# Kernel optimization log

Measured on AMD Instinct MI355X. Metric: run time of the kernel, lower is better.

The kernel has to match this reference:

```python
import jax, jax.numpy as jnp
import numpy as np

N = 100000      # num_nodes
E = 1600000     # num_edges
D_IN = 256      # input_dim
H = 64          # hidden_dim
OUT = 32        # output_dim
EMB = 128       # node2vec embedding_dim
HEADS = 2       # GAT heads (concat=False -> mean over heads)
NEG_SLOPE = 0.2 # GATConv leaky_relu default


def setup_inputs() -> dict:
    key = jax.random.key(0)
    ks = jax.random.split(key, 24)
    s = lambda k, shape, fan: (jax.random.normal(k, shape, jnp.float32) * (1.0 / np.sqrt(fan)))
    return {
        "x": jax.random.normal(ks[0], (N, D_IN), jnp.float32),
        "edge_index": jax.random.randint(ks[1], (2, E), 0, N, jnp.int64),
        # frozen node2vec embedding table (used under no_grad in the original)
        "n2v_emb": jax.random.normal(ks[2], (N, EMB), jnp.float32),
        "n2v_proj_w": s(ks[3], (EMB, H), EMB), "n2v_proj_b": jnp.zeros((H,), jnp.float32),
        "input_proj_w": s(ks[4], (D_IN + H, H), D_IN + H), "input_proj_b": jnp.zeros((H,), jnp.float32),
        "gate_w": s(ks[5], (D_IN + H, H), D_IN + H), "gate_b": jnp.zeros((H,), jnp.float32),
        # SAGEConv layers: out = mean_agg(x_j) @ wl + bl + x @ wr
        "sage0_wl": s(ks[6], (H, H), H), "sage0_bl": jnp.zeros((H,), jnp.float32), "sage0_wr": s(ks[7], (H, H), H),
        "sage1_wl": s(ks[8], (H, H), H), "sage1_bl": jnp.zeros((H,), jnp.float32), "sage1_wr": s(ks[9], (H, H), H),
        # GATConv(H, H, heads=2, concat=False)
        "gat_w": s(ks[10], (H, HEADS * H), H),
        "gat_att_src": s(ks[11], (HEADS, H), H), "gat_att_dst": s(ks[12], (HEADS, H), H),
        "gat_b": jnp.zeros((H,), jnp.float32),
        "fin_wl": s(ks[13], (H, OUT), H), "fin_bl": jnp.zeros((OUT,), jnp.float32), "fin_wr": s(ks[14], (H, OUT), H),
    }


def _sage(h, src, dst, wl, bl, wr, n):
    # PyG SAGEConv with mean aggregation: lin_l(mean_j h_j) + lin_r(h_i)
    msum = jax.ops.segment_sum(h[src], dst, num_segments=n)
    deg = jax.ops.segment_sum(jnp.ones((src.shape[0],), h.dtype), dst, num_segments=n)
    agg = msum / jnp.maximum(deg, 1.0)[:, None]
    return agg @ wl + bl + h @ wr


def _gat(h, src, dst, w, att_src, att_dst, b, n):
    # GATConv with self-loops (PyG default), heads averaged (concat=False)
    loops = jnp.arange(n, dtype=src.dtype)
    src = jnp.concatenate([src, loops]); dst = jnp.concatenate([dst, loops])
    xh = (h @ w).reshape(n, HEADS, H)                     # [n, heads, H]
    a_src = jnp.einsum('nhd,hd->nh', xh, att_src)         # [n, heads]
    a_dst = jnp.einsum('nhd,hd->nh', xh, att_dst)
    e = jax.nn.leaky_relu(a_src[src] + a_dst[dst], NEG_SLOPE)  # [E', heads]
    emax = jax.ops.segment_max(e, dst, num_segments=n)
    ex = jnp.exp(e - emax[dst])
    esum = jax.ops.segment_sum(ex, dst, num_segments=n)
    alpha = ex / (esum[dst] + 1e-16)                      # edge softmax per dst, per head
    out = jax.ops.segment_sum(alpha[:, :, None] * xh[src], dst, num_segments=n)
    return out.mean(axis=1) + b                           # [n, H]


def reference(x, edge_index, n2v_emb, n2v_proj_w, n2v_proj_b, input_proj_w, input_proj_b,
              gate_w, gate_b, sage0_wl, sage0_bl, sage0_wr, sage1_wl, sage1_bl, sage1_wr,
              gat_w, gat_att_src, gat_att_dst, gat_b, fin_wl, fin_bl, fin_wr):
    n = x.shape[0]
    src, dst = edge_index[0], edge_index[1]
    # node2vec embeddings are frozen (torch.no_grad in original)
    n2v = jax.lax.stop_gradient(n2v_emb)
    n2v_p = n2v @ n2v_proj_w + n2v_proj_b                 # [n, H]
    combined = jnp.concatenate([x, n2v_p], axis=-1)       # [n, D_IN+H]
    gate = jax.nn.sigmoid(combined @ gate_w + gate_b)
    x_proj = combined @ input_proj_w + input_proj_b
    raw_proj = jnp.concatenate([x, jnp.zeros((n, H), x.dtype)], axis=-1) @ input_proj_w + input_proj_b
    h = gate * x_proj + (1.0 - gate) * raw_proj           # node_indices=None -> all nodes
    h = jax.nn.relu(_sage(h, src, dst, sage0_wl, sage0_bl, sage0_wr, n))
    h = jax.nn.relu(_sage(h, src, dst, sage1_wl, sage1_bl, sage1_wr, n))
    h = jax.nn.relu(_gat(h, src, dst, gat_w, gat_att_src, gat_att_dst, gat_b, n))
    return _sage(h, src, dst, fin_wl, fin_bl, fin_wr, n)  # [n, OUT]
```

## Files before the change

kernel.cpp:

```cpp
#include <hip/hip_runtime.h>
#include <math.h>

#define NN 100000
#define NE 1600000
#define DIN 256
#define HD 64
#define OUTD 32
#define EMBD 128
#define SLOPE 0.2f
#define AST 68
#define NT ((NN + 63) / 64)
#define SCHUNK 1024
#define SNBLK ((NN + SCHUNK - 1) / SCHUNK)
#define FCH 25000
#define FNC ((NE + FCH - 1) / FCH)

typedef __attribute__((ext_vector_type(8))) short bf16x8;
typedef __attribute__((ext_vector_type(8))) unsigned short u16x8;
typedef __attribute__((ext_vector_type(4))) float f32x4;

__device__ __forceinline__ float lrelu(float x) { return x > 0.f ? x : SLOPE * x; }
__device__ __forceinline__ ushort f2b(float f) {
    unsigned u = __float_as_uint(f);
    return (ushort)((u + 0x7FFFu + ((u >> 16) & 1u)) >> 16);
}
__device__ __forceinline__ float b2f(ushort v) { return __uint_as_float(((unsigned)v) << 16); }

__global__ void k_count(const int* __restrict__ dst, int* __restrict__ cnt) {
    int i = blockIdx.x * blockDim.x + threadIdx.x;
    if (i < NE) atomicAdd(&cnt[dst[i]], 1);
}

__global__ __launch_bounds__(256) void k_scan1(const int* __restrict__ cnt,
                                               int* __restrict__ rowptr,
                                               int* __restrict__ blksum) {
    __shared__ int ts[256];
    int base = blockIdx.x * SCHUNK + threadIdx.x * 4;
    int v0 = 0, v1 = 0, v2 = 0, v3 = 0;
    if (base < NN)     v0 = cnt[base];
    if (base + 1 < NN) v1 = cnt[base + 1];
    if (base + 2 < NN) v2 = cnt[base + 2];
    if (base + 3 < NN) v3 = cnt[base + 3];
    int s = v0 + v1 + v2 + v3;
    ts[threadIdx.x] = s;
    __syncthreads();
    for (int off = 1; off < 256; off <<= 1) {
        int w = (threadIdx.x >= off) ? ts[threadIdx.x - off] : 0;
        __syncthreads();
        ts[threadIdx.x] += w;
        __syncthreads();
    }
    int excl = ts[threadIdx.x] - s;
    if (base < NN)     rowptr[base]     = excl;
    if (base + 1 < NN) rowptr[base + 1] = excl + v0;
    if (base + 2 < NN) rowptr[base + 2] = excl + v0 + v1;
    if (base + 3 < NN) rowptr[base + 3] = excl + v0 + v1 + v2;
    if (threadIdx.x == 255) blksum[blockIdx.x] = ts[255];
}

__global__ __launch_bounds__(128) void k_scan2(int* __restrict__ blksum) {
    __shared__ int ts[128];
    int t = threadIdx.x;
    int v = (t < SNBLK) ? blksum[t] : 0;
    ts[t] = v;
    __syncthreads();
    for (int off = 1; off < 128; off <<= 1) {
        int w = (t >= off) ? ts[t - off] : 0;
        __syncthreads();
        ts[t] += w;
        __syncthreads();
    }
    if (t < SNBLK) blksum[t] = ts[t] - v;
}

__global__ void k_scan3(const int* __restrict__ blksum, const int* __restrict__ cnt,
                        int* __restrict__ rowptr, int* __restrict__ cursor,
                        float* __restrict__ invdeg) {
    int i = blockIdx.x * blockDim.x + threadIdx.x;
    if (i < NN) {
        int v = rowptr[i] + blksum[i >> 10];
        rowptr[i] = v;
        cursor[i] = v;
        invdeg[i] = 1.0f / fmaxf((float)cnt[i], 1.0f);
    }
    if (i == 0) rowptr[NN] = NE;
}

__global__ __launch_bounds__(256) void k_fill_x(const int* __restrict__ src,
                                                const int* __restrict__ dst,
                                                int* __restrict__ cursor,
                                                int* __restrict__ colsrc) {
    int xcd = blockIdx.x & 7;
    int chunk = blockIdx.x >> 3;
    int lo = xcd * (NN / 8);
    int hi = (xcd == 7) ? NN : lo + (NN / 8);
    int beg = chunk * FCH;
    int end = min(beg + FCH, NE);
    for (int i = beg + (int)threadIdx.x; i < end; i += 256) {
        int d = dst[i];
        if (d >= lo && d < hi) {
            int pos = atomicAdd(&cursor[d], 1);
            colsrc[pos] = src[i];
        }
    }
}

__device__ __forceinline__ void stageA(const float* __restrict__ g, int nbase, int ldg, int koff,
                                       float (*As)[AST]) {
    for (int i = threadIdx.x; i < 1024; i += 256) {
        int m = i >> 4, k4 = (i & 15) << 2;
        int row = nbase + m;
        if (row >= NN) row = NN - 1;
        *(float4*)&As[m][k4] = *(const float4*)&g[(size_t)row * ldg + koff + k4];
    }
}
__device__ __forceinline__ void stageW(const float* __restrict__ g, float* Ws) {
    for (int i = threadIdx.x; i < 1024; i += 256) ((float4*)Ws)[i] = ((const float4*)g)[i];
}
__device__ __forceinline__ void stageWcols(const float* __restrict__ g, int ldg, int coff,
                                           float* Ws) {
    for (int i = threadIdx.x; i < 1024; i += 256) {
        int r = i >> 4, c4 = (i & 15) << 2;
        *(float4*)&Ws[r * 64 + c4] = *(const float4*)&g[r * ldg + coff + c4];
    }
}
__device__ __forceinline__ void mac16v(const float (*As)[AST], const float* __restrict__ Ws,
                                       float (*acc)[4], int tr, int tc) {
#pragma unroll 4
    for (int k4 = 0; k4 < 64; k4 += 4) {
        float4 a0 = *(const float4*)&As[tr * 4 + 0][k4];
        float4 a1 = *(const float4*)&As[tr * 4 + 1][k4];
        float4 a2 = *(const float4*)&As[tr * 4 + 2][k4];
        float4 a3 = *(const float4*)&As[tr * 4 + 3][k4];
#pragma unroll
        for (int j = 0; j < 4; j++) {
            float4 w = *(const float4*)&Ws[(k4 + j) * 64 + tc * 4];
            float e0 = (&a0.x)[j], e1 = (&a1.x)[j], e2 = (&a2.x)[j], e3 = (&a3.x)[j];
            acc[0][0] += e0 * w.x; acc[0][1] += e0 * w.y; acc[0][2] += e0 * w.z; acc[0][3] += e0 * w.w;
            acc[1][0] += e1 * w.x; acc[1][1] += e1 * w.y; acc[1][2] += e1 * w.z; acc[1][3] += e1 * w.w;
            acc[2][0] += e2 * w.x; acc[2][1] += e2 * w.y; acc[2][2] += e2 * w.z; acc[2][3] += e2 * w.w;
            acc[3][0] += e3 * w.x; acc[3][1] += e3 * w.y; acc[3][2] += e3 * w.z; acc[3][3] += e3 * w.w;
        }
    }
}

__global__ __launch_bounds__(256) void k_n2vp_t(const float* __restrict__ n2v,
                                                const float* __restrict__ w,
                                                const float* __restrict__ b,
                                                float* __restrict__ n2vp) {
    __shared__ float As[64][AST];
    __shared__ float Ws[64 * 64];
    int nbase = blockIdx.x * 64;
    int tc = threadIdx.x & 15, tr = threadIdx.x >> 4;
    float acc[4][4] = {};
    for (int c = 0; c < 2; c++) {
        if (c) __syncthreads();
        stageA(n2v, nbase, EMBD, c * 64, As);
        stageW(w + c * 64 * 64, Ws);
        __syncthreads();
        mac16v(As, Ws, acc, tr, tc);
    }
    float b0 = b[tc * 4], b1 = b[tc * 4 + 1], b2 = b[tc * 4 + 2], b3 = b[tc * 4 + 3];
#pragma unroll
    for (int i = 0; i < 4; i++) {
        int row = nbase + tr * 4 + i;
        if (row < NN) {
            float4 o = {acc[i][0] + b0, acc[i][1] + b1, acc[i][2] + b2, acc[i][3] + b3};
            *(float4*)&n2vp[(size_t)row * HD + tc * 4] = o;
        }
    }
}

__global__ __launch_bounds__(256) void k_front_t(const float* __restrict__ x,
                                                 const float* __restrict__ n2vp,
                                                 const float* __restrict__ ip_w,
                                                 const float* __restrict__ ip_b,
                                                 const float* __restrict__ gate_w,
                                                 const float* __restrict__ gate_b,
                                                 float* __restrict__ h0,
                                                 ushort* __restrict__ h0b) {
    __shared__ ushort Ah[64][40], Al[64][40];
    __shared__ ushort Bih[64][40], Bil[64][40];
    __shared__ ushort Bgh[64][40], Bgl[64][40];
    int nbase = blockIdx.x * 64;
    int tid = threadIdx.x;
    int w = tid >> 6, l = tid & 63;
    int lr = l & 15, lg = l >> 4, lk = lg * 8;
    f32x4 zero = {0.f, 0.f, 0.f, 0.f};
    f32x4 araw[4], ag[4], adel[4];
#pragma unroll
    for (int t = 0; t < 4; t++) { araw[t] = zero; ag[t] = zero; adel[t] = zero; }

    int arow = tid >> 2, ak0 = (tid & 3) << 3;
    int garow = nbase + arow;
    if (garow >= NN) garow = NN - 1;

    for (int c = 0; c < 8; c++) {
        if (c) __syncthreads();
        {
            const float* src = &x[(size_t)garow * DIN + c * 32 + ak0];
            u16x8 th, tl;
#pragma unroll
            for (int u = 0; u < 8; u++) {
                float v = src[u];
                ushort h = f2b(v);
                th[u] = h;
                tl[u] = f2b(v - b2f(h));
            }
            *(u16x8*)&Ah[arow][ak0] = th;
            *(u16x8*)&Al[arow][ak0] = tl;
        }
        {
            const float* pi = &ip_w[(size_t)(c * 32 + w * 8) * 64 + l];
            const float* pg = &gate_w[(size_t)(c * 32 + w * 8) * 64 + l];
            u16x8 ih, il, gh, gl2;
#pragma unroll
            for (int u = 0; u < 8; u++) {
                float v = pi[u * 64];
                ushort h = f2b(v);
                ih[u] = h; il[u] = f2b(v - b2f(h));
                float g = pg[u * 64];
                ushort hg = f2b(g);
                gh[u] = hg; gl2[u] = f2b(g - b2f(hg));
            }
            *(u16x8*)&Bih[l][w * 8] = ih;
            *(u16x8*)&Bil[l][w * 8] = il;
            *(u16x8*)&Bgh[l][w * 8] = gh;
            *(u16x8*)&Bgl[l][w * 8] = gl2;
        }
        __syncthreads();
        bf16x8 ah = *(const bf16x8*)&Ah[w * 16 + lr][lk];
        bf16x8 al = *(const bf16x8*)&Al[w * 16 + lr][lk];
#pragma unroll
        for (int t = 0; t < 4; t++) {
            int col = t * 16 + lr;
            bf16x8 bih = *(const bf16x8*)&Bih[col][lk];
            bf16x8 bil = *(const bf16x8*)&Bil[col][lk];
            bf16x8 bgh = *(const bf16x8*)&Bgh[col][lk];
            bf16x8 bgl = *(const bf16x8*)&Bgl[col][lk];
            f32x4 r = araw[t];
            r = __builtin_amdgcn_mfma_f32_16x16x32_bf16(ah, bih, r, 0, 0, 0);
            r = __builtin_amdgcn_mfma_f32_16x16x32_bf16(ah, bil, r, 0, 0, 0);
            r = __builtin_amdgcn_mfma_f32_16x16x32_bf16(al, bih, r, 0, 0, 0);
            araw[t] = r;
            f32x4 g = ag[t];
            g = __builtin_amdgcn_mfma_f32_16x16x32_bf16(ah, bgh, g, 0, 0, 0);
            g = __builtin_amdgcn_mfma_f32_16x16x32_bf16(ah, bgl, g, 0, 0, 0);
            g = __builtin_amdgcn_mfma_f32_16x16x32_bf16(al, bgh, g, 0, 0, 0);
            ag[t] = g;
        }
    }
    for (int c = 0; c < 2; c++) {
        __syncthreads();
        {
            const float* src = &n2vp[(size_t)garow * HD + c * 32 + ak0];
            u16x8 th, tl;
#pragma unroll
            for (int u = 0; u < 8; u++) {
                float v = src[u];
                ushort h = f2b(v);
                th[u] = h;
                tl[u] = f2b(v - b2f(h));
            }
            *(u16x8*)&Ah[arow][ak0] = th;
            *(u16x8*)&Al[arow][ak0] = tl;
        }
        {
            const float* pi = &ip_w[(size_t)(DIN + c * 32 + w * 8) * 64 + l];
            const float* pg = &gate_w[(size_t)(DIN + c * 32 + w * 8) * 64 + l];
            u16x8 ih, il, gh, gl2;
#pragma unroll
            for (int u = 0; u < 8; u++) {
                float v = pi[u * 64];
                ushort h = f2b(v);
                ih[u] = h; il[u] = f2b(v - b2f(h));
                float g = pg[u * 64];
                ushort hg = f2b(g);
                gh[u] = hg; gl2[u] = f2b(g - b2f(hg));
            }
            *(u16x8*)&Bih[l][w * 8] = ih;
            *(u16x8*)&Bil[l][w * 8] = il;
            *(u16x8*)&Bgh[l][w * 8] = gh;
            *(u16x8*)&Bgl[l][w * 8] = gl2;
        }
        __syncthreads();
        bf16x8 ah = *(const bf16x8*)&Ah[w * 16 + lr][lk];
        bf16x8 al = *(const bf16x8*)&Al[w * 16 + lr][lk];
#pragma unroll
        for (int t = 0; t < 4; t++) {
            int col = t * 16 + lr;
            bf16x8 bih = *(const bf16x8*)&Bih[col][lk];
            bf16x8 bil = *(const bf16x8*)&Bil[col][lk];
            bf16x8 bgh = *(const bf16x8*)&Bgh[col][lk];
            bf16x8 bgl = *(const bf16x8*)&Bgl[col][lk];
            f32x4 r = adel[t];
            r = __builtin_amdgcn_mfma_f32_16x16x32_bf16(ah, bih, r, 0, 0, 0);
            r = __builtin_amdgcn_mfma_f32_16x16x32_bf16(ah, bil, r, 0, 0, 0);
            r = __builtin_amdgcn_mfma_f32_16x16x32_bf16(al, bih, r, 0, 0, 0);
            adel[t] = r;
            f32x4 g = ag[t];
            g = __builtin_amdgcn_mfma_f32_16x16x32_bf16(ah, bgh, g, 0, 0, 0);
            g = __builtin_amdgcn_mfma_f32_16x16x32_bf16(ah, bgl, g, 0, 0, 0);
            g = __builtin_amdgcn_mfma_f32_16x16x32_bf16(al, bgh, g, 0, 0, 0);
            ag[t] = g;
        }
    }
#pragma unroll
    for (int t = 0; t < 4; t++) {
        int col = t * 16 + lr;
        float ib = ip_b[col], gb2 = gate_b[col];
#pragma unroll
        for (int r = 0; r < 4; r++) {
            int row = nbase + w * 16 + lg * 4 + r;
            if (row < NN) {
                float raw = araw[t][r] + ib;
                float sg = 1.f / (1.f + __expf(-(ag[t][r] + gb2)));
                float o = raw + sg * adel[t][r];
                h0[(size_t)row * HD + col] = o;
                h0b[(size_t)row * HD + col] = f2b(o);
            }
        }
    }
}

__global__ void k_gather_mean(const int* __restrict__ rowptr, const int* __restrict__ colsrc,
                              const float* __restrict__ invdeg, const ushort* __restrict__ hb,
                              float* __restrict__ agg) {
    int t = threadIdx.x & 63;
    int lane = t & 31, half = t >> 5;
    int gw = blockIdx.x * (blockDim.x >> 6) + (threadIdx.x >> 6);
    int stride = gridDim.x * (blockDim.x >> 6);
    for (int n = gw; n < NN; n += stride) {
        int bg = rowptr[n], en = rowptr[n + 1];
        float a0 = 0.f, a1 = 0.f;
        int i = bg + half;
        for (; i + 6 < en; i += 8) {
            int sa = colsrc[i], sb = colsrc[i + 2], sc = colsrc[i + 4], sd = colsrc[i + 6];
            ushort2 va = *(const ushort2*)&hb[(size_t)sa * HD + lane * 2];
            ushort2 vb = *(const ushort2*)&hb[(size_t)sb * HD + lane * 2];
            ushort2 vc = *(const ushort2*)&hb[(size_t)sc * HD + lane * 2];
            ushort2 vd = *(const ushort2*)&hb[(size_t)sd * HD + lane * 2];
            a0 += b2f(va.x) + b2f(vb.x) + b2f(vc.x) + b2f(vd.x);
            a1 += b2f(va.y) + b2f(vb.y) + b2f(vc.y) + b2f(vd.y);
        }
        for (; i < en; i += 2) {
            int s = colsrc[i];
            ushort2 v = *(const ushort2*)&hb[(size_t)s * HD + lane * 2];
            a0 += b2f(v.x);
            a1 += b2f(v.y);
        }
        a0 += __shfl_xor(a0, 32);
        a1 += __shfl_xor(a1, 32);
        if (half == 0) {
            float id = invdeg[n];
            float2 o = {a0 * id, a1 * id};
            *(float2*)&agg[(size_t)n * HD + lane * 2] = o;
        }
    }
}

__global__ __launch_bounds__(256) void k_sage_t(const float* __restrict__ agg,
                                                const float* __restrict__ h,
                                                const float* __restrict__ wl,
                                                const float* __restrict__ bl,
                                                const float* __restrict__ wr,
                                                float* __restrict__ hout,
                                                ushort* __restrict__ houtb) {
    __shared__ float As[64][AST];
    __shared__ float Ws[64 * 64];
    int nbase = blockIdx.x * 64;
    int tc = threadIdx.x & 15, tr = threadIdx.x >> 4;
    float acc[4][4] = {};
    stageA(agg, nbase, HD, 0, As);
    stageW(wl, Ws);
    __syncthreads();
    mac16v(As, Ws, acc, tr, tc);
    __syncthreads();
    stageA(h, nbase, HD, 0, As);
    stageW(wr, Ws);
    __syncthreads();
    mac16v(As, Ws, acc, tr, tc);
    float b0 = bl[tc * 4], b1 = bl[tc * 4 + 1], b2 = bl[tc * 4 + 2], b3 = bl[tc * 4 + 3];
#pragma unroll
    for (int i = 0; i < 4; i++) {
        int row = nbase + tr * 4 + i;
        if (row < NN) {
            float4 o = {fmaxf(acc[i][0] + b0, 0.f), fmaxf(acc[i][1] + b1, 0.f),
                        fmaxf(acc[i][2] + b2, 0.f), fmaxf(acc[i][3] + b3, 0.f)};
            *(float4*)&hout[(size_t)row * HD + tc * 4] = o;
            ushort4 ob = {f2b(o.x), f2b(o.y), f2b(o.z), f2b(o.w)};
            *(ushort4*)&houtb[(size_t)row * HD + tc * 4] = ob;
        }
    }
}

__global__ __launch_bounds__(256) void k_gatxh_t(const float* __restrict__ h,
                                                 const float* __restrict__ w,
                                                 const float* __restrict__ att_s,
                                                 const float* __restrict__ att_d,
                                                 ushort* __restrict__ xhb,
                                                 float* __restrict__ a_s,
                                                 float* __restrict__ a_d) {
    __shared__ float As[64][AST];
    __shared__ float Ws[64 * 64];
    int nbase = blockIdx.x * 64;
    int tc = threadIdx.x & 15, tr = threadIdx.x >> 4;
    stageA(h, nbase, HD, 0, As);
#pragma unroll
    for (int half = 0; half < 2; half++) {
        if (half) __syncthreads();
        stageWcols(w, 128, half * 64, Ws);
        __syncthreads();
        float acc[4][4] = {};
        mac16v(As, Ws, acc, tr, tc);
        float as0 = att_s[half * 64 + tc * 4], as1 = att_s[half * 64 + tc * 4 + 1];
        float as2 = att_s[half * 64 + tc * 4 + 2], as3 = att_s[half * 64 + tc * 4 + 3];
        float ad0 = att_d[half * 64 + tc * 4], ad1 = att_d[half * 64 + tc * 4 + 1];
        float ad2 = att_d[half * 64 + tc * 4 + 2], ad3 = att_d[half * 64 + tc * 4 + 3];
#pragma unroll
        for (int i = 0; i < 4; i++) {
            int row = nbase + tr * 4 + i;
            float ps = acc[i][0] * as0 + acc[i][1] * as1 + acc[i][2] * as2 + acc[i][3] * as3;
            float pd = acc[i][0] * ad0 + acc[i][1] * ad1 + acc[i][2] * ad2 + acc[i][3] * ad3;
#pragma unroll
            for (int off = 8; off; off >>= 1) {
                ps += __shfl_xor(ps, off);
                pd += __shfl_xor(pd, off);
            }
            if (row < NN) {
                ushort4 ob = {f2b(acc[i][0]), f2b(acc[i][1]), f2b(acc[i][2]), f2b(acc[i][3])};
                *(ushort4*)&xhb[(size_t)row * 128 + half * 64 + tc * 4] = ob;
                if (tc == 0) {
                    a_s[row * 2 + half] = ps;
                    a_d[row * 2 + half] = pd;
                }
            }
        }
    }
}

__global__ void k_gat_fused(const int* __restrict__ rowptr, const int* __restrict__ colsrc,
                            const float* __restrict__ a_s, const float* __restrict__ a_d,
                            const ushort* __restrict__ xhb, const float* __restrict__ gb,
                            float* __restrict__ hout) {
    int t = threadIdx.x & 63;
    int lane = t & 31, half = t >> 5;
    int bl4 = (lane & 15) * 4;
    float4 bias4 = *(const float4*)&gb[bl4];
    int gw = blockIdx.x * (blockDim.x >> 6) + (threadIdx.x >> 6);
    int stride = gridDim.x * (blockDim.x >> 6);
    for (int n = gw; n < NN; n += stride) {
        int bg = rowptr[n], en = rowptr[n + 1];
        float ad0 = a_d[n * 2], ad1 = a_d[n * 2 + 1];
        float a0 = 0.f, a1 = 0.f, a2 = 0.f, a3 = 0.f;
        float ss0 = 0.f, ss1 = 0.f;
        int i = bg + half;
        for (; i + 2 < en; i += 4) {
            int sa = colsrc[i], sb = colsrc[i + 2];
            float2 ava = *(const float2*)&a_s[sa * 2];
            float2 avb = *(const float2*)&a_s[sb * 2];
            ushort4 xva = *(const ushort4*)&xhb[(size_t)sa * 128 + lane * 4];
            ushort4 xvb = *(const ushort4*)&xhb[(size_t)sb * 128 + lane * 4];
            float wa0 = __expf(lrelu(ava.x + ad0));
            float wa1 = __expf(lrelu(ava.y + ad1));
            float wb0 = __expf(lrelu(avb.x + ad0));
            float wb1 = __expf(lrelu(avb.y + ad1));
            ss0 += wa0 + wb0;
            ss1 += wa1 + wb1;
            float wsa = (lane < 16) ? wa0 : wa1;
            float wsb = (lane < 16) ? wb0 : wb1;
            a0 += wsa * b2f(xva.x) + wsb * b2f(xvb.x);
            a1 += wsa * b2f(xva.y) + wsb * b2f(xvb.y);
            a2 += wsa * b2f(xva.z) + wsb * b2f(xvb.z);
            a3 += wsa * b2f(xva.w) + wsb * b2f(xvb.w);
        }
        for (; i < en; i += 2) {
            int s = colsrc[i];
            float2 av = *(const float2*)&a_s[s * 2];
            float w0 = __expf(lrelu(av.x + ad0));
            float w1 = __expf(lrelu(av.y + ad1));
            ss0 += w0;
            ss1 += w1;
            float wsel = (lane < 16) ? w0 : w1;
            ushort4 xv = *(const ushort4*)&xhb[(size_t)s * 128 + lane * 4];
            a0 += wsel * b2f(xv.x);
            a1 += wsel * b2f(xv.y);
            a2 += wsel * b2f(xv.z);
            a3 += wsel * b2f(xv.w);
        }
        if (half == 0) {
            float2 av = *(const float2*)&a_s[n * 2];
            float w0 = __expf(lrelu(av.x + ad0));
            float w1 = __expf(lrelu(av.y + ad1));
            ss0 += w0;
            ss1 += w1;
            float wsel = (lane < 16) ? w0 : w1;
            ushort4 xv = *(const ushort4*)&xhb[(size_t)n * 128 + lane * 4];
            a0 += wsel * b2f(xv.x);
            a1 += wsel * b2f(xv.y);
            a2 += wsel * b2f(xv.z);
            a3 += wsel * b2f(xv.w);
        }
        ss0 += __shfl_xor(ss0, 32);
        ss1 += __shfl_xor(ss1, 32);
        a0 += __shfl_xor(a0, 32);
        a1 += __shfl_xor(a1, 32);
        a2 += __shfl_xor(a2, 32);
        a3 += __shfl_xor(a3, 32);
        float r = (lane < 16) ? (0.5f / (ss0 + 1e-16f)) : (0.5f / (ss1 + 1e-16f));
        float v0 = a0 * r, v1 = a1 * r, v2 = a2 * r, v3 = a3 * r;
        float p0 = __shfl_xor(v0, 16);
        float p1 = __shfl_xor(v1, 16);
        float p2 = __shfl_xor(v2, 16);
        float p3 = __shfl_xor(v3, 16);
        if (half == 0 && lane < 16) {
            float4 o = {fmaxf(v0 + p0 + bias4.x, 0.f), fmaxf(v1 + p1 + bias4.y, 0.f),
                        fmaxf(v2 + p2 + bias4.z, 0.f), fmaxf(v3 + p3 + bias4.w, 0.f)};
            *(float4*)&hout[(size_t)n * HD + lane * 4] = o;
        }
    }
}

__global__ void k_pfin(const float* __restrict__ h, const float* __restrict__ wl,
                       ushort* __restrict__ Pb) {
    __shared__ float sw[HD * OUTD];
    for (int i = threadIdx.x; i < HD * OUTD; i += blockDim.x) sw[i] = wl[i];
    __syncthreads();
    int t = threadIdx.x & 63;
    int c = t & 31, half = t >> 5;
    int gw = blockIdx.x * (blockDim.x >> 6) + (threadIdx.x >> 6);
    int stride = gridDim.x * (blockDim.x >> 6);
    for (int n = gw; n < NN; n += stride) {
        float hv = h[(size_t)n * HD + t];
        float acc = 0.f;
#pragma unroll 8
        for (int i = 0; i < 32; i++) {
            float bb = __shfl(hv, half * 32 + i);
            acc += bb * sw[half * 1024 + i * 32 + c];
        }
        acc += __shfl_xor(acc, 32);
        if (half == 0) Pb[(size_t)n * OUTD + c] = f2b(acc);
    }
}

__global__ void k_final_fused(const int* __restrict__ rowptr, const int* __restrict__ colsrc,
                              const float* __restrict__ invdeg, const ushort* __restrict__ Pb,
                              const float* __restrict__ h, const float* __restrict__ bl,
                              const float* __restrict__ wr, float* __restrict__ out) {
    __shared__ float sw[HD * OUTD];
    for (int i = threadIdx.x; i < HD * OUTD; i += blockDim.x) sw[i] = wr[i];
    __syncthreads();
    int t = threadIdx.x & 63;
    int j = t & 31, half = t >> 5;
    int quarter = t >> 4, lane16 = t & 15;
    float bias = bl[j];
    int gw = blockIdx.x * (blockDim.x >> 6) + (threadIdx.x >> 6);
    int stride = gridDim.x * (blockDim.x >> 6);
    for (int n = gw; n < NN; n += stride) {
        int bg = rowptr[n], en = rowptr[n + 1];
        float a0 = 0.f, a1 = 0.f;
        int i = bg + quarter;
        for (; i + 4 < en; i += 8) {
            int sa = colsrc[i], sb = colsrc[i + 4];
            ushort2 va = *(const ushort2*)&Pb[(size_t)sa * OUTD + lane16 * 2];
            ushort2 vb = *(const ushort2*)&Pb[(size_t)sb * OUTD + lane16 * 2];
            a0 += b2f(va.x) + b2f(vb.x);
            a1 += b2f(va.y) + b2f(vb.y);
        }
        for (; i < en; i += 4) {
            int s = colsrc[i];
            ushort2 v = *(const ushort2*)&Pb[(size_t)s * OUTD + lane16 * 2];
            a0 += b2f(v.x);
            a1 += b2f(v.y);
        }
        a0 += __shfl_xor(a0, 32);
        a1 += __shfl_xor(a1, 32);
        a0 += __shfl_xor(a0, 16);
        a1 += __shfl_xor(a1, 16);
        float hv = h[(size_t)n * HD + t];
        float o = 0.f;
#pragma unroll 8
        for (int i2 = 0; i2 < 32; i2++) {
            float bb = __shfl(hv, half * 32 + i2);
            o += bb * sw[half * 1024 + i2 * 32 + j];
        }
        o += __shfl_xor(o, 32);
        float ga = __shfl(a0, j >> 1);
        float gb_ = __shfl(a1, j >> 1);
        float gv = (j & 1) ? gb_ : ga;
        if (half == 0) out[(size_t)n * OUTD + j] = gv * invdeg[n] + bias + o;
    }
}

extern "C" void kernel_launch(void* const* d_in, const int* in_sizes, int n_in,
                              void* d_out, int out_size, void* d_ws, size_t ws_size,
                              hipStream_t stream) {
    const float* x      = (const float*)d_in[0];
    const int*   eidx   = (const int*)d_in[1];
    const float* n2v    = (const float*)d_in[2];
    const float* n2v_w  = (const float*)d_in[3];
    const float* n2v_b  = (const float*)d_in[4];
    const float* ip_w   = (const float*)d_in[5];
    const float* ip_b   = (const float*)d_in[6];
    const float* gate_w = (const float*)d_in[7];
    const float* gate_b = (const float*)d_in[8];
    const float* s0_wl  = (const float*)d_in[9];
    const float* s0_bl  = (const float*)d_in[10];
    const float* s0_wr  = (const float*)d_in[11];
    const float* s1_wl  = (const float*)d_in[12];
    const float* s1_bl  = (const float*)d_in[13];
    const float* s1_wr  = (const float*)d_in[14];
    const float* gat_w  = (const float*)d_in[15];
    const float* att_s  = (const float*)d_in[16];
    const float* att_d  = (const float*)d_in[17];
    const float* gat_b  = (const float*)d_in[18];
    const float* f_wl   = (const float*)d_in[19];
    const float* f_bl   = (const float*)d_in[20];
    const float* f_wr   = (const float*)d_in[21];

    const int* src = eidx;
    const int* dst = eidx + NE;

    float*  ws     = (float*)d_ws;
    float*  invdeg = ws;
    float*  S1     = invdeg + NN;
    float*  S2     = S1 + (size_t)NN * HD;
    float*  SA     = S2 + (size_t)NN * HD;
    float*  a_s    = SA + (size_t)NN * HD;
    float*  a_d    = a_s + (size_t)NN * 2;
    ushort* Pb     = (ushort*)(a_d + (size_t)NN * 2);
    ushort* hb     = Pb + (size_t)NN * OUTD;
    ushort* xhb    = hb + (size_t)NN * HD;
    int*    cnt    = (int*)(xhb + (size_t)NN * 128);
    int*    rowptr = cnt + NN;
    int*    cursor = rowptr + NN + 1;
    int*    blksum = cursor + NN;
    int*    colsrc = blksum + 128;

    float* n2vp = SA;
    float* agg  = SA;
    float* out  = (float*)d_out;

    const int BT = 256;
    dim3 b128(128), b256(BT);
    int eblk = (NE + BT - 1) / BT;
    int nblk = (NN + BT - 1) / BT;

    hipMemsetAsync(cnt, 0, (size_t)NN * 4, stream);
    k_count<<<eblk, b256, 0, stream>>>(dst, cnt);
    k_scan1<<<SNBLK, b256, 0, stream>>>(cnt, rowptr, blksum);
    k_scan2<<<1, b128, 0, stream>>>(blksum);
    k_scan3<<<nblk, b256, 0, stream>>>(blksum, cnt, rowptr, cursor, invdeg);
    k_fill_x<<<8 * FNC, b256, 0, stream>>>(src, dst, cursor, colsrc);

    k_n2vp_t<<<NT, b256, 0, stream>>>(n2v, n2v_w, n2v_b, n2vp);
    k_front_t<<<NT, b256, 0, stream>>>(x, n2vp, ip_w, ip_b, gate_w, gate_b, S2, hb);

    k_gather_mean<<<2048, b256, 0, stream>>>(rowptr, colsrc, invdeg, hb, agg);
    k_sage_t<<<NT, b256, 0, stream>>>(agg, S2, s0_wl, s0_bl, s0_wr, S1, hb);

    k_gather_mean<<<2048, b256, 0, stream>>>(rowptr, colsrc, invdeg, hb, agg);
    k_sage_t<<<NT, b256, 0, stream>>>(agg, S1, s1_wl, s1_bl, s1_wr, S2, hb);

    k_gatxh_t<<<NT, b256, 0, stream>>>(S2, gat_w, att_s, att_d, xhb, a_s, a_d);
    k_gat_fused<<<2048, b256, 0, stream>>>(rowptr, colsrc, a_s, a_d, xhb, gat_b, S1);

    k_pfin<<<2048, b256, 0, stream>>>(S1, f_wl, Pb);
    k_final_fused<<<2048, b256, 0, stream>>>(rowptr, colsrc, invdeg, Pb, S1, f_bl, f_wr, out);
}
```

Measured before the change: 695.7 us.

## Fuse node2vec projection and CSR fill into a single front kernel launch

Removes the separate n2v projection kernel by computing it with split-bf16 MFMA inside the front kernel and keeping the result in registers. That result is then staged straight into shared memory, so the n2vp intermediate is never written to or read back from global memory. The CSR fill blocks are appended to the same grid, so the atomic scatter can overlap with the front-end GEMM work and one launch is saved. The costs are extra registers for the held projection and a precision change from fp32 FMA to three-term bf16 MFMA for the projection.

```diff
diff --git a/kernel.cpp b/kernel.cpp
--- a/kernel.cpp
+++ b/kernel.cpp
@@ -86,25 +86,6 @@
     if (i == 0) rowptr[NN] = NE;
 }
 
-__global__ __launch_bounds__(256) void k_fill_x(const int* __restrict__ src,
-                                                const int* __restrict__ dst,
-                                                int* __restrict__ cursor,
-                                                int* __restrict__ colsrc) {
-    int xcd = blockIdx.x & 7;
-    int chunk = blockIdx.x >> 3;
-    int lo = xcd * (NN / 8);
-    int hi = (xcd == 7) ? NN : lo + (NN / 8);
-    int beg = chunk * FCH;
-    int end = min(beg + FCH, NE);
-    for (int i = beg + (int)threadIdx.x; i < end; i += 256) {
-        int d = dst[i];
-        if (d >= lo && d < hi) {
-            int pos = atomicAdd(&cursor[d], 1);
-            colsrc[pos] = src[i];
-        }
-    }
-}
-
 __device__ __forceinline__ void stageA(const float* __restrict__ g, int nbase, int ldg, int koff,
                                        float (*As)[AST]) {
     for (int i = threadIdx.x; i < 1024; i += 256) {
@@ -144,65 +125,107 @@
     }
 }
 
-__global__ __launch_bounds__(256) void k_n2vp_t(const float* __restrict__ n2v,
-                                                const float* __restrict__ w,
-                                                const float* __restrict__ b,
-                                                float* __restrict__ n2vp) {
-    __shared__ float As[64][AST];
-    __shared__ float Ws[64 * 64];
-    int nbase = blockIdx.x * 64;
-    int tc = threadIdx.x & 15, tr = threadIdx.x >> 4;
-    float acc[4][4] = {};
-    for (int c = 0; c < 2; c++) {
-        if (c) __syncthreads();
-        stageA(n2v, nbase, EMBD, c * 64, As);
-        stageW(w + c * 64 * 64, Ws);
-        __syncthreads();
-        mac16v(As, Ws, acc, tr, tc);
-    }
-    float b0 = b[tc * 4], b1 = b[tc * 4 + 1], b2 = b[tc * 4 + 2], b3 = b[tc * 4 + 3];
-#pragma unroll
-    for (int i = 0; i < 4; i++) {
-        int row = nbase + tr * 4 + i;
-        if (row < NN) {
-            float4 o = {acc[i][0] + b0, acc[i][1] + b1, acc[i][2] + b2, acc[i][3] + b3};
-            *(float4*)&n2vp[(size_t)row * HD + tc * 4] = o;
-        }
-    }
-}
-
-__global__ __launch_bounds__(256) void k_front_t(const float* __restrict__ x,
-                                                 const float* __restrict__ n2vp,
-                                                 const float* __restrict__ ip_w,
-                                                 const float* __restrict__ ip_b,
-                                                 const float* __restrict__ gate_w,
-                                                 const float* __restrict__ gate_b,
-                                                 float* __restrict__ h0,
-                                                 ushort* __restrict__ h0b) {
+__global__ __launch_bounds__(256) void k_megafront(
+        const float* __restrict__ x, const float* __restrict__ n2v,
+        const float* __restrict__ n2v_w, const float* __restrict__ n2v_b,
+        const float* __restrict__ ip_w, const float* __restrict__ ip_b,
+        const float* __restrict__ gate_w, const float* __restrict__ gate_b,
+        float* __restrict__ h0, ushort* __restrict__ h0b,
+        const int* __restrict__ esrc, const int* __restrict__ edst,
+        int* __restrict__ cursor, int* __restrict__ colsrc) {
     __shared__ ushort Ah[64][40], Al[64][40];
     __shared__ ushort Bih[64][40], Bil[64][40];
     __shared__ ushort Bgh[64][40], Bgl[64][40];
+
+    if (blockIdx.x >= NT) {
+        int fb = blockIdx.x - NT;
+        int cls = blockIdx.x & 7;
+        int chunk = fb >> 3;
+        int lo = cls * (NN / 8);
+        int hi = (cls == 7) ? NN : lo + (NN / 8);
+        int beg = chunk * FCH;
+        int end = min(beg + FCH, NE);
+        for (int i = beg + (int)threadIdx.x; i < end; i += 256) {
+            int d = edst[i];
+            if (d >= lo && d < hi) {
+                int pos = atomicAdd(&cursor[d], 1);
+                colsrc[pos] = esrc[i];
+            }
+        }
+        return;
+    }
+
     int nbase = blockIdx.x * 64;
     int tid = threadIdx.x;
     int w = tid >> 6, l = tid & 63;
     int lr = l & 15, lg = l >> 4, lk = lg * 8;
     f32x4 zero = {0.f, 0.f, 0.f, 0.f};
-    f32x4 araw[4], ag[4], adel[4];
-#pragma unroll
-    for (int t = 0; t < 4; t++) { araw[t] = zero; ag[t] = zero; adel[t] = zero; }
+    f32x4 araw[4], ag[4], adel[4], pn[4];
+#pragma unroll
+    for (int t = 0; t < 4; t++) { araw[t] = zero; ag[t] = zero; adel[t] = zero; pn[t] = zero; }
 
     int arow = tid >> 2, ak0 = (tid & 3) << 3;
     int garow = nbase + arow;
     if (garow >= NN) garow = NN - 1;
 
-    for (int c = 0; c < 8; c++) {
+    for (int c = 0; c < 4; c++) {
         if (c) __syncthreads();
         {
-            const float* src = &x[(size_t)garow * DIN + c * 32 + ak0];
+            const float* ap = &n2v[(size_t)garow * EMBD + c * 32 + ak0];
             u16x8 th, tl;
 #pragma unroll
             for (int u = 0; u < 8; u++) {
-                float v = src[u];
+                float v = ap[u];
+                ushort h = f2b(v);
+                th[u] = h;
+                tl[u] = f2b(v - b2f(h));
+            }
+            *(u16x8*)&Ah[arow][ak0] = th;
+            *(u16x8*)&Al[arow][ak0] = tl;
+        }
+        {
+            const float* pw = &n2v_w[(size_t)(c * 32 + w * 8) * 64 + l];
+            u16x8 ih, il;
+#pragma unroll
+            for (int u = 0; u < 8; u++) {
+                float v = pw[u * 64];
+                ushort h = f2b(v);
+                ih[u] = h;
+                il[u] = f2b(v - b2f(h));
+            }
+            *(u16x8*)&Bih[l][w * 8] = ih;
+            *(u16x8*)&Bil[l][w * 8] = il;
+        }
+        __syncthreads();
+        bf16x8 ah = *(const bf16x8*)&Ah[w * 16 + lr][lk];
+        bf16x8 al = *(const bf16x8*)&Al[w * 16 + lr][lk];
+#pragma unroll
+        for (int t = 0; t < 4; t++) {
+            int col = t * 16 + lr;
+            bf16x8 bih = *(const bf16x8*)&Bih[col][lk];
+            bf16x8 bil = *(const bf16x8*)&Bil[col][lk];
+            f32x4 r = pn[t];
+            r = __builtin_amdgcn_mfma_f32_16x16x32_bf16(ah, bih, r, 0, 0, 0);
+            r = __builtin_amdgcn_mfma_f32_16x16x32_bf16(ah, bil, r, 0, 0, 0);
+            r = __builtin_amdgcn_mfma_f32_16x16x32_bf16(al, bih, r, 0, 0, 0);
+            pn[t] = r;
+        }
+    }
+#pragma unroll
+    for (int t = 0; t < 4; t++) {
+        float nb = n2v_b[t * 16 + lr];
+#pragma unroll
+        for (int r = 0; r < 4; r++) pn[t][r] += nb;
+    }
+
+    for (int c = 0; c < 8; c++) {
+        __syncthreads();
+        {
+            const float* ap = &x[(size_t)garow * DIN + c * 32 + ak0];
+            u16x8 th, tl;
+#pragma unroll
+            for (int u = 0; u < 8; u++) {
+                float v = ap[u];
                 ushort h = f2b(v);
                 th[u] = h;
                 tl[u] = f2b(v - b2f(h));
@@ -250,20 +273,21 @@
             ag[t] = g;
         }
     }
+
     for (int c = 0; c < 2; c++) {
         __syncthreads();
-        {
-            const float* src = &n2vp[(size_t)garow * HD + c * 32 + ak0];
-            u16x8 th, tl;
-#pragma unroll
-            for (int u = 0; u < 8; u++) {
-                float v = src[u];
+#pragma unroll
+        for (int tt = 0; tt < 2; tt++) {
+            int t = c * 2 + tt;
+            int ak = tt * 16 + lr;
+#pragma unroll
+            for (int r = 0; r < 4; r++) {
+                int row = w * 16 + lg * 4 + r;
+                float v = pn[t][r];
                 ushort h = f2b(v);
-                th[u] = h;
-                tl[u] = f2b(v - b2f(h));
-            }
-            *(u16x8*)&Ah[arow][ak0] = th;
-            *(u16x8*)&Al[arow][ak0] = tl;
+                Ah[row][ak] = h;
+                Al[row][ak] = f2b(v - b2f(h));
+            }
         }
         {
             const float* pi = &ip_w[(size_t)(DIN + c * 32 + w * 8) * 64 + l];
@@ -637,9 +661,8 @@
     int*    blksum = cursor + NN;
     int*    colsrc = blksum + 128;
 
-    float* n2vp = SA;
-    float* agg  = SA;
-    float* out  = (float*)d_out;
+    float* agg = SA;
+    float* out = (float*)d_out;
 
     const int BT = 256;
     dim3 b128(128), b256(BT);
@@ -651,10 +674,10 @@
     k_scan1<<<SNBLK, b256, 0, stream>>>(cnt, rowptr, blksum);
     k_scan2<<<1, b128, 0, stream>>>(blksum);
     k_scan3<<<nblk, b256, 0, stream>>>(blksum, cnt, rowptr, cursor, invdeg);
-    k_fill_x<<<8 * FNC, b256, 0, stream>>>(src, dst, cursor, colsrc);
-
-    k_n2vp_t<<<NT, b256, 0, stream>>>(n2v, n2v_w, n2v_b, n2vp);
-    k_front_t<<<NT, b256, 0, stream>>>(x, n2vp, ip_w, ip_b, gate_w, gate_b, S2, hb);
+
+    k_megafront<<<NT + 8 * FNC, b256, 0, stream>>>(x, n2v, n2v_w, n2v_b, ip_w, ip_b,
+                                                   gate_w, gate_b, S2, hb,
+                                                   src, dst, cursor, colsrc);
 
     k_gather_mean<<<2048, b256, 0, stream>>>(rowptr, colsrc, invdeg, hb, agg);
     k_sage_t<<<NT, b256, 0, stream>>>(agg, S2, s0_wl, s0_bl, s0_wr, S1, hb);
```

Result: faster. 670.9 us (-3.6%).
